# Optimization experiments

Hardware: AMD Instinct MI355X
Metric: run time of the kernel (lower is better)

Reference implementation:

```python
import jax, jax.numpy as jnp
import numpy as np

B, S, E, D = 256, 256, 2, 128  # batch, seq_len, encoder_dim, decoder_dim


def setup_inputs() -> dict:
    key = jax.random.key(0)
    ks = jax.random.split(key, 9)
    u = lambda k, shape, n: jax.random.uniform(k, shape, jnp.float32, -1.0 / np.sqrt(n), 1.0 / np.sqrt(n))
    return {
        "out_encoder": jax.random.normal(ks[0], (B, S, E), jnp.float32),
        "W1_w": u(ks[1], (S, S), S),            # Linear(seq_len, seq_len)
        "W1_b": u(ks[2], (S,), S),
        "W2_w": u(ks[3], (S, 2 * S), 2 * S),    # Linear(2*seq_len, seq_len)
        "W2_b": u(ks[4], (S,), 2 * S),
        "W_ih": u(ks[5], (4 * D, E), D),        # LSTMCell input weights (i,f,g,o)
        "W_hh": u(ks[6], (4 * D, D), D),
        "b_ih": u(ks[7], (4 * D,), D),
        "b_hh": u(ks[8], (4 * D,), D),
    }


def reference(out_encoder, W1_w, W1_b, W2_w, W2_b, W_ih, W_hh, b_ih, b_hh):
    b, s, e = out_encoder.shape
    d = W_hh.shape[1]
    dt = out_encoder.dtype

    # W_2 term: encoder flattened to [B, 2S]; identical every step, hoist it.
    w2term = out_encoder.reshape(b, s * e) @ W2_w.T + W2_b          # [B, S]
    # W_1 applied to a row of S copies of h_d equals h_d * rowsum(W1) + b.
    w1sum = W1_w.sum(axis=1)                                        # [S]

    def attn(h):  # h: [B, D] -> context [B, E]
        hterm = h[:, :, None] * w1sum[None, None, :] + W1_b         # [B, D, S]
        en = jnp.tanh(w2term[:, None, :] + hterm)                   # [B, D, S]
        alpha = jax.nn.softmax(en, axis=-1).mean(axis=1)            # [B, S] (softmax over seq)
        return jnp.einsum('bs,bse->be', alpha, out_encoder)         # [B, E]

    def lstm_cell(x, h, c):
        gates = x @ W_ih.T + h @ W_hh.T + b_ih + b_hh               # [B, 4D]
        i, f, g, o = jnp.split(gates, 4, axis=-1)
        c = jax.nn.sigmoid(f) * c + jax.nn.sigmoid(i) * jnp.tanh(g)
        h = jax.nn.sigmoid(o) * jnp.tanh(c)
        return h, c

    h0 = jnp.zeros((b, d), dt)
    c0 = jnp.zeros((b, d), dt)

    def step(carry, _):
        h, c = carry
        x = attn(h)
        h, c = lstm_cell(x, h, c)
        return (h, c), h

    _, hs = jax.lax.scan(step, (h0, c0), None, length=s)
    return hs  # [S, B, D]: stacked decoder hidden states (original returns a list of h_t)
```

## Files before the change

### kernel.cpp

```cpp
#include <hip/hip_runtime.h>

#define NB 256
#define NS 256
#define NE 2
#define ND 128
#define NT 512
#define NN 16
#define RING 32
#define SLOT 144

typedef float vf4 __attribute__((ext_vector_type(4)));

constexpr float L2E = 1.4426950408889634f;
constexpr float PI_F = 3.14159265358979323846f;

template <int C>
__device__ __forceinline__ float dppadd(float x) {
    return x + __builtin_bit_cast(float,
        __builtin_amdgcn_update_dpp(0, __builtin_bit_cast(int, x), C, 0xF, 0xF, true));
}
__device__ __forceinline__ float red_quad(float x) {
    x = dppadd<0xB1>(x); x = dppadd<0x4E>(x); return x;
}
__device__ __forceinline__ float red_oct(float x) {
    x = dppadd<0xB1>(x); x = dppadd<0x4E>(x); x = dppadd<0x141>(x); return x;
}
__device__ __forceinline__ float red_wave64(float x) {
    x = dppadd<0xB1>(x); x = dppadd<0x4E>(x); x = dppadd<0x141>(x);
    x = dppadd<0x140>(x); x = dppadd<0x142>(x); x = dppadd<0x143>(x); return x;
}
__device__ __forceinline__ float red_half32(float x) {
    x = dppadd<0xB1>(x); x = dppadd<0x4E>(x); x = dppadd<0x141>(x);
    x = dppadd<0x140>(x); x = dppadd<0x142>(x); return x;
}
__device__ __forceinline__ float red_grp16(float x) {
    x = dppadd<0x141>(x); x = dppadd<0x140>(x);
    x = dppadd<0x142>(x); x = dppadd<0x143>(x); return x;
}

__global__ __launch_bounds__(NT, 2)
void attn_lstm_decoder(const float* __restrict__ enc,
                       const float* __restrict__ W1w,
                       const float* __restrict__ W1b,
                       const float* __restrict__ W2w,
                       const float* __restrict__ W2b,
                       const float* __restrict__ Wih,
                       const float* __restrict__ Whh,
                       const float* __restrict__ bih,
                       const float* __restrict__ bhh,
                       float* __restrict__ out)
{
    const int b    = blockIdx.x;
    const int t    = threadIdx.x;
    const int wave = t >> 6;
    const int lane = t & 63;
    const int g    = t >> 2;
    const int q    = t & 3;
    const int half = lane >> 5;
    const int idx  = lane & 31;
    const int jnode = 2 * wave + half;

    __shared__ __align__(16) float hist[RING * SLOT];
    __shared__ __align__(16) float xwbuf[2][16];
    __shared__ float A2_l[NS];
    __shared__ float g2_l[NS];
    __shared__ float e0_l[NS];
    __shared__ float e1_l[NS];
    __shared__ float Ml[NN * NN];
    __shared__ float2 Pn[NN];
    __shared__ float2 Vl[NN];

    {
        float v = enc[b * (NS * NE) + t];
        if (t & 1) e1_l[t >> 1] = v; else e0_l[t >> 1] = v;
    }
    if (t < NN * NN) {
        const int mi = t >> 4, mj = t & 15;
        const float w = (mi == 0) ? (1.0f / NN) : (2.0f / NN);
        Ml[t] = w * __cosf((float)(mi * (2 * mj + 1)) * (PI_F / (2 * NN)));
    }
    __syncthreads();

    for (int r = 0; r < 32; ++r) {
        const int s = wave * 32 + r;
        float p = W1w[s * NS + lane]       + W1w[s * NS + lane + 64]
                + W1w[s * NS + lane + 128] + W1w[s * NS + lane + 192];
        p = red_wave64(p);
        if (lane == 63) g2_l[s] = p * (2.0f * L2E);
        float qq = 0.0f;
        #pragma unroll
        for (int kk = 0; kk < 8; ++kk) {
            const int c = lane + kk * 64;
            const float ev = (c & 1) ? e1_l[c >> 1] : e0_l[c >> 1];
            qq = fmaf(ev, W2w[s * (2 * NS) + c], qq);
        }
        qq = red_wave64(qq);
        if (lane == 63) A2_l[s] = (qq + W2b[s] + W1b[s]) * (2.0f * L2E);
    }
    __syncthreads();

    {
        const float y  = __cosf((float)(2 * jnode + 1) * (PI_F / (2 * NN)));
        const float C2 = -2.0f * L2E;
        float l = 0.0f, p0 = 0.0f, p1 = 0.0f;
        #pragma unroll
        for (int k = 0; k < 8; ++k) {
            const int s = k * 32 + idx;
            const float m1 = fmaf(y, g2_l[s], A2_l[s]);
            const float u  = __builtin_amdgcn_exp2f(m1);
            const float rc = __builtin_amdgcn_rcpf(u + 1.0f);
            const float e  = __builtin_amdgcn_exp2f(rc * C2);
            l += e;
            p0 = fmaf(e, e0_l[s], p0);
            p1 = fmaf(e, e1_l[s], p1);
        }
        l = red_half32(l); p0 = red_half32(p0); p1 = red_half32(p1);
        if ((lane & 31) == 31) {
            const float rl = __builtin_amdgcn_rcpf(l);
            Pn[jnode] = make_float2(p0 * rl, p1 * rl);
        }
    }
    __syncthreads();

    if (t < NN) {
        float v0 = 0.0f, v1 = 0.0f;
        #pragma unroll
        for (int j = 0; j < NN; ++j) {
            v0 = fmaf(Ml[t * NN + j], Pn[j].x, v0);
            v1 = fmaf(Ml[t * NN + j], Pn[j].y, v1);
        }
        Vl[t] = make_float2(v0 * (1.0f / ND), v1 * (1.0f / ND));
    }

    vf4 wr[4][8];
    float wi0_[4], wi1_[4], bb_[4];
    #pragma unroll
    for (int j = 0; j < 4; ++j) {
        const int r = g + 128 * j;
        const vf4* W4 = reinterpret_cast<const vf4*>(Whh + r * ND + q * 32);
        #pragma unroll
        for (int i = 0; i < 8; ++i) wr[j][i] = W4[i];
        wi0_[j] = Wih[r * 2 + 0];
        wi1_[j] = Wih[r * 2 + 1];
        bb_[j]  = bih[r] + bhh[r];
    }

    if (t < ND) hist[31 * SLOT + 36 * (t >> 5) + (t & 31)] = 0.0f;
    float h_reg = 0.0f, c_reg = 0.0f;
    __syncthreads();

    float V0r[NN], V1r[NN];
    #pragma unroll
    for (int i = 0; i < NN; ++i) { V0r[i] = Vl[i].x; V1r[i] = Vl[i].y; }

    auto phaseG = [&](float h, int pw) {
        float acc0 = fmaf(V0r[1], h, V0r[0]);
        float acc1 = fmaf(V1r[1], h, V1r[0]);
        float tp = 1.0f, tc = h;
        const float h2 = h + h;
        #pragma unroll
        for (int i = 2; i < NN; ++i) {
            const float tn = fmaf(h2, tc, -tp);
            acc0 = fmaf(V0r[i], tn, acc0);
            acc1 = fmaf(V1r[i], tn, acc1);
            tp = tc; tc = tn;
        }
        acc0 = red_grp16(acc0);
        acc1 = red_grp16(acc1);
        if (lane == 63) {
            xwbuf[pw][2 * wave + 0] = acc0;
            xwbuf[pw][2 * wave + 1] = acc1;
        }
    };

    phaseG(0.0f, 0);
    __syncthreads();

    for (int step = 0; step < NS; ++step) {
        const int pr = step & 1;
        const int rs = (step + RING - 1) & (RING - 1);
        const int ws = step & (RING - 1);

        if ((step & 15) == 0 && step > 0) {
            const int sb  = (step - 16) & (RING - 1);
            const int k   = t >> 5;
            const int l32 = t & 31;
            const int w   = 4 * l32;
            const vf4 v = *reinterpret_cast<const vf4*>(
                &hist[(sb + k) * SLOT + 36 * (w >> 5) + (w & 31)]);
            *reinterpret_cast<vf4*>(
                &out[(size_t)(step - 16 + k) * (NB * ND) + b * ND + w]) = v;
        }

        float2 xv = *reinterpret_cast<const float2*>(&xwbuf[pr][2 * (lane & 7)]);
        float x0 = red_oct(xv.x);
        float x1 = red_oct(xv.y);

        const vf4* hb = reinterpret_cast<const vf4*>(&hist[rs * SLOT]) + 9 * q;
        vf4 a0 = {0.f,0.f,0.f,0.f}, a1 = a0, a2 = a0, a3 = a0;
        #pragma unroll
        for (int i = 0; i < 8; ++i) {
            const vf4 hv = hb[i];
            a0 = __builtin_elementwise_fma(wr[0][i], hv, a0);
            a1 = __builtin_elementwise_fma(wr[1][i], hv, a1);
            a2 = __builtin_elementwise_fma(wr[2][i], hv, a2);
            a3 = __builtin_elementwise_fma(wr[3][i], hv, a3);
        }
        float d0 = (a0.x + a0.y) + (a0.z + a0.w);
        float d1 = (a1.x + a1.y) + (a1.z + a1.w);
        float d2 = (a2.x + a2.y) + (a2.z + a2.w);
        float d3 = (a3.x + a3.y) + (a3.z + a3.w);
        d0 = red_quad(d0);  d1 = red_quad(d1);
        d2 = red_quad(d2);  d3 = red_quad(d3);

        const float gi = d0 + fmaf(x0, wi0_[0], fmaf(x1, wi1_[0], bb_[0]));
        const float gf = d1 + fmaf(x0, wi0_[1], fmaf(x1, wi1_[1], bb_[1]));
        const float gg = d2 + fmaf(x0, wi0_[2], fmaf(x1, wi1_[2], bb_[2]));
        const float go = d3 + fmaf(x0, wi0_[3], fmaf(x1, wi1_[3], bb_[3]));

        const float si = __builtin_amdgcn_rcpf(1.0f + __builtin_amdgcn_exp2f(-L2E * gi));
        const float sf = __builtin_amdgcn_rcpf(1.0f + __builtin_amdgcn_exp2f(-L2E * gf));
        const float so = __builtin_amdgcn_rcpf(1.0f + __builtin_amdgcn_exp2f(-L2E * go));
        const float tg = 1.0f - 2.0f * __builtin_amdgcn_rcpf(__builtin_amdgcn_exp2f(2.0f * L2E * gg) + 1.0f);
        c_reg = sf * c_reg + si * tg;
        const float tc2 = 1.0f - 2.0f * __builtin_amdgcn_rcpf(__builtin_amdgcn_exp2f(2.0f * L2E * c_reg) + 1.0f);
        h_reg = so * tc2;

        if (q == 0) hist[ws * SLOT + 36 * (g >> 5) + (g & 31)] = h_reg;
        phaseG(h_reg, pr ^ 1);

        __syncthreads();
    }

    {
        const int k   = t >> 5;
        const int l32 = t & 31;
        const int w   = 4 * l32;
        const vf4 v = *reinterpret_cast<const vf4*>(
            &hist[(16 + k) * SLOT + 36 * (w >> 5) + (w & 31)]);
        *reinterpret_cast<vf4*>(
            &out[(size_t)(240 + k) * (NB * ND) + b * ND + w]) = v;
    }
}

extern "C" void kernel_launch(void* const* d_in, const int* in_sizes, int n_in,
                              void* d_out, int out_size, void* d_ws, size_t ws_size,
                              hipStream_t stream) {
    const float* enc = (const float*)d_in[0];
    const float* W1w = (const float*)d_in[1];
    const float* W1b = (const float*)d_in[2];
    const float* W2w = (const float*)d_in[3];
    const float* W2b = (const float*)d_in[4];
    const float* Wih = (const float*)d_in[5];
    const float* Whh = (const float*)d_in[6];
    const float* bih = (const float*)d_in[7];
    const float* bhh = (const float*)d_in[8];
    attn_lstm_decoder<<<NB, NT, 0, stream>>>(enc, W1w, W1b, W2w, W2b,
                                             Wih, Whh, bih, bhh, (float*)d_out);
}
```

Before: 318.1 us.

## Convert Chebyshev context evaluation to monomial Horner split across quad lanes

Converts the Chebyshev coefficients of the attention context polynomial into monomial coefficients once per block. Each quad lane then evaluates a quarter of the polynomial with a short Horner chain in h^4 and the results are summed by a quad reduction. This replaces the 15-term serial recurrence on the per-step critical path. It also hoists the LDS loads of h history and xwbuf above the periodic output store so they issue earlier. Monomial coefficients of a degree-15 Chebyshev expansion can be large, which risks floating-point cancellation.

```diff
diff --git a/kernel.cpp b/kernel.cpp
--- a/kernel.cpp
+++ b/kernel.cpp
@@ -13,6 +13,24 @@
 
 constexpr float L2E = 1.4426950408889634f;
 constexpr float PI_F = 3.14159265358979323846f;
+
+__device__ const float CT[16][16] = {
+ {1,0,0,0,0,0,0,0,0,0,0,0,0,0,0,0},
+ {0,1,0,0,0,0,0,0,0,0,0,0,0,0,0,0},
+ {-1,0,2,0,0,0,0,0,0,0,0,0,0,0,0,0},
+ {0,-3,0,4,0,0,0,0,0,0,0,0,0,0,0,0},
+ {1,0,-8,0,8,0,0,0,0,0,0,0,0,0,0,0},
+ {0,5,0,-20,0,16,0,0,0,0,0,0,0,0,0,0},
+ {-1,0,18,0,-48,0,32,0,0,0,0,0,0,0,0,0},
+ {0,-7,0,56,0,-112,0,64,0,0,0,0,0,0,0,0},
+ {1,0,-32,0,160,0,-256,0,128,0,0,0,0,0,0,0},
+ {0,9,0,-120,0,432,0,-576,0,256,0,0,0,0,0,0},
+ {-1,0,50,0,-400,0,1120,0,-1280,0,512,0,0,0,0,0},
+ {0,-11,0,220,0,-1232,0,2816,0,-2816,0,1024,0,0,0,0},
+ {1,0,-72,0,840,0,-3584,0,6912,0,-6144,0,2048,0,0,0},
+ {0,13,0,-364,0,2912,0,-9984,0,16640,0,-13312,0,4096,0,0},
+ {-1,0,98,0,-1568,0,9408,0,-26880,0,39424,0,-28672,0,8192,0},
+ {0,-15,0,560,0,-6048,0,28800,0,-70400,0,92160,0,-61440,0,16384}};
 
 template <int C>
 __device__ __forceinline__ float dppadd(float x) {
@@ -56,6 +74,8 @@
     const int lane = t & 63;
     const int g    = t >> 2;
     const int q    = t & 3;
+    const bool qb0 = q & 1;
+    const bool qb1 = q & 2;
     const int half = lane >> 5;
     const int idx  = lane & 31;
     const int jnode = 2 * wave + half;
@@ -69,6 +89,7 @@
     __shared__ float Ml[NN * NN];
     __shared__ float2 Pn[NN];
     __shared__ float2 Vl[NN];
+    __shared__ float Pm0[NN], Pm1[NN];
 
     {
         float v = enc[b * (NS * NE) + t];
@@ -149,27 +170,39 @@
     float h_reg = 0.0f, c_reg = 0.0f;
     __syncthreads();
 
-    float V0r[NN], V1r[NN];
+    if (t < NN) {
+        float s0 = 0.0f, s1 = 0.0f;
+        #pragma unroll
+        for (int k = 0; k < NN; ++k) {
+            s0 = fmaf(Vl[k].x, CT[k][t], s0);
+            s1 = fmaf(Vl[k].y, CT[k][t], s1);
+        }
+        Pm0[t] = s0; Pm1[t] = s1;
+    }
+    __syncthreads();
+
+    float Q0[4], Q1[4];
     #pragma unroll
-    for (int i = 0; i < NN; ++i) { V0r[i] = Vl[i].x; V1r[i] = Vl[i].y; }
+    for (int i = 0; i < 4; ++i) { Q0[i] = Pm0[4 * i + q]; Q1[i] = Pm1[4 * i + q]; }
 
     auto phaseG = [&](float h, int pw) {
-        float acc0 = fmaf(V0r[1], h, V0r[0]);
-        float acc1 = fmaf(V1r[1], h, V1r[0]);
-        float tp = 1.0f, tc = h;
-        const float h2 = h + h;
-        #pragma unroll
-        for (int i = 2; i < NN; ++i) {
-            const float tn = fmaf(h2, tc, -tp);
-            acc0 = fmaf(V0r[i], tn, acc0);
-            acc1 = fmaf(V1r[i], tn, acc1);
-            tp = tc; tc = tn;
-        }
-        acc0 = red_grp16(acc0);
-        acc1 = red_grp16(acc1);
+        const float h2 = h * h;
+        const float h3 = h2 * h;
+        const float h4 = h2 * h2;
+        const float hq = qb1 ? (qb0 ? h3 : h2) : (qb0 ? h : 1.0f);
+        float a0 = fmaf(Q0[3], h4, Q0[2]);
+        a0 = fmaf(a0, h4, Q0[1]);
+        a0 = fmaf(a0, h4, Q0[0]);
+        float a1 = fmaf(Q1[3], h4, Q1[2]);
+        a1 = fmaf(a1, h4, Q1[1]);
+        a1 = fmaf(a1, h4, Q1[0]);
+        a0 *= hq;
+        a1 *= hq;
+        a0 = red_quad(a0);  a1 = red_quad(a1);
+        a0 = red_grp16(a0); a1 = red_grp16(a1);
         if (lane == 63) {
-            xwbuf[pw][2 * wave + 0] = acc0;
-            xwbuf[pw][2 * wave + 1] = acc1;
+            xwbuf[pw][2 * wave + 0] = a0;
+            xwbuf[pw][2 * wave + 1] = a1;
         }
     };
 
@@ -180,6 +213,12 @@
         const int pr = step & 1;
         const int rs = (step + RING - 1) & (RING - 1);
         const int ws = step & (RING - 1);
+
+        float2 xv = *reinterpret_cast<const float2*>(&xwbuf[pr][2 * (lane & 7)]);
+        const vf4* hb = reinterpret_cast<const vf4*>(&hist[rs * SLOT]) + 9 * q;
+        vf4 hv[8];
+        #pragma unroll
+        for (int i = 0; i < 8; ++i) hv[i] = hb[i];
 
         if ((step & 15) == 0 && step > 0) {
             const int sb  = (step - 16) & (RING - 1);
@@ -192,19 +231,16 @@
                 &out[(size_t)(step - 16 + k) * (NB * ND) + b * ND + w]) = v;
         }
 
-        float2 xv = *reinterpret_cast<const float2*>(&xwbuf[pr][2 * (lane & 7)]);
         float x0 = red_oct(xv.x);
         float x1 = red_oct(xv.y);
 
-        const vf4* hb = reinterpret_cast<const vf4*>(&hist[rs * SLOT]) + 9 * q;
         vf4 a0 = {0.f,0.f,0.f,0.f}, a1 = a0, a2 = a0, a3 = a0;
         #pragma unroll
         for (int i = 0; i < 8; ++i) {
-            const vf4 hv = hb[i];
-            a0 = __builtin_elementwise_fma(wr[0][i], hv, a0);
-            a1 = __builtin_elementwise_fma(wr[1][i], hv, a1);
-            a2 = __builtin_elementwise_fma(wr[2][i], hv, a2);
-            a3 = __builtin_elementwise_fma(wr[3][i], hv, a3);
+            a0 = __builtin_elementwise_fma(wr[0][i], hv[i], a0);
+            a1 = __builtin_elementwise_fma(wr[1][i], hv[i], a1);
+            a2 = __builtin_elementwise_fma(wr[2][i], hv[i], a2);
+            a3 = __builtin_elementwise_fma(wr[3][i], hv[i], a3);
         }
         float d0 = (a0.x + a0.y) + (a0.z + a0.w);
         float d1 = (a1.x + a1.y) + (a1.z + a1.w);
```

Result: faster. 308.6 us (-3.0%).
